# Kernel optimization log

Measured on AMD Instinct MI355X. Metric: run time of the kernel, lower is better.

The kernel has to match this reference:

```python
import jax, jax.numpy as jnp
import numpy as np

BLOCK_NUM = 64
B, M, K, N = 4, 4096, 4096, 4096  # batch, rows, in_features, out_features


def setup_inputs() -> dict:
    key = jax.random.key(0)
    k1, k2 = jax.random.split(key)
    x = jax.random.normal(k1, (B, M, K), dtype=jnp.float32)
    weight = jax.random.normal(k2, (K, N), dtype=jnp.float32) * 0.02
    return {"x": x, "weight": weight}


def reference(x, weight):
    # Block-local matmul: output block (i, j) = A_block(i, j) @ W_block(i, j).
    # No cross-block reduction: each (i, j) output block depends on exactly one
    # A block and one W block. Vectorized as a single einsum over all blocks.
    b, m, k = x.shape
    k2, n = weight.shape
    Bn = BLOCK_NUM
    r, c, o = m // Bn, k // Bn, n // Bn  # per-block rows / contract / cols
    A = x.reshape(b, Bn, r, Bn, c)        # [b, i, r, j, c]
    W = weight.reshape(Bn, c, Bn, o)      # [i, c, j, o] (rows split by i, cols by j)
    out = jnp.einsum('birjc,icjo->birjo', A, W)
    return out.reshape(b, m, n)
```

## Files before the change

### kernel.cpp

```cpp
#include <hip/hip_runtime.h>
#include <hip/hip_bf16.h>


typedef short bf16x8 __attribute__((ext_vector_type(8)));
typedef float f32x4 __attribute__((ext_vector_type(4)));

__device__ __forceinline__ unsigned short f2bf(float f) {
    union { float f; unsigned int u; } v; v.f = f;
    unsigned int u = v.u;
    u += 0x7fffu + ((u >> 16) & 1u);
    return (unsigned short)(u >> 16);
}

__global__ __launch_bounds__(256, 4) void block_matmul_kernel(
    const float* __restrict__ x, const float* __restrict__ w,
    float* __restrict__ out) {
    __shared__ char smem[32768];
    unsigned short* Ws = reinterpret_cast<unsigned short*>(smem + 16384);
    float*          Os = reinterpret_cast<float*>(smem);

    const int chunk = 8192 >> 3;
    int orig = blockIdx.x;
    int wg   = (orig & 7) * chunk + (orig >> 3);

    int b = wg >> 11;
    int i = (wg >> 5) & 63;
    int q = wg & 31;

    const float* Ab = x   + ((size_t)(b * 4096 + i * 64)) * 4096 + q * 128;
    const float* Wb = w   + ((size_t)(i * 64)) * 4096 + q * 128;
    float*       Ob = out + ((size_t)(b * 4096 + i * 64)) * 4096 + q * 128;

    const int t = threadIdx.x;

    float4 va[8];
    #pragma unroll
    for (int it = 0; it < 8; ++it) {
        int idx = it * 256 + t;
        int m   = idx >> 5;
        int k4  = (idx & 31) << 2;
        va[it] = *reinterpret_cast<const float4*>(Ab + (size_t)m * 4096 + k4);
    }
    const int n  = t & 127;
    const int c0 = (t >> 7) << 2;
    float wv[32];
    #pragma unroll
    for (int it = 0; it < 8; ++it) {
        int c = it * 8 + c0;
        #pragma unroll
        for (int r = 0; r < 4; ++r)
            wv[it * 4 + r] = Wb[(size_t)(c + r) * 4096 + n];
    }

    #pragma unroll
    for (int it = 0; it < 8; ++it) {
        int idx = it * 256 + t;
        int m   = idx >> 5;
        int k4  = (idx & 31) << 2;
        unsigned long long pk =
            (unsigned long long)f2bf(va[it].x)         |
            ((unsigned long long)f2bf(va[it].y) << 16) |
            ((unsigned long long)f2bf(va[it].z) << 32) |
            ((unsigned long long)f2bf(va[it].w) << 48);
        int addr = m * 256 + ((k4 * 2) ^ ((m & 7) << 4));
        *reinterpret_cast<unsigned long long*>(smem + addr) = pk;
    }
    #pragma unroll
    for (int it = 0; it < 8; ++it) {
        int c = it * 8 + c0;
        unsigned long long pk =
            (unsigned long long)f2bf(wv[it * 4 + 0])         |
            ((unsigned long long)f2bf(wv[it * 4 + 1]) << 16) |
            ((unsigned long long)f2bf(wv[it * 4 + 2]) << 32) |
            ((unsigned long long)f2bf(wv[it * 4 + 3]) << 48);
        int addr = n * 128 + ((c * 2) ^ ((n & 7) << 4));
        *reinterpret_cast<unsigned long long*>(
            reinterpret_cast<char*>(Ws) + addr) = pk;
    }

    __syncthreads();

    const int l  = t & 63;
    const int wvid = t >> 6;
    const int lr = l & 15;
    const int lk = l >> 4;

    f32x4 acc[8];
    #pragma unroll
    for (int z = 0; z < 8; ++z) acc[z] = (f32x4){0.f, 0.f, 0.f, 0.f};

    const int am = wvid * 16 + lr;
    #pragma unroll
    for (int jj = 0; jj < 2; ++jj) {
        #pragma unroll
        for (int kt = 0; kt < 2; ++kt) {
            int kbA = jj * 128 + kt * 64 + lk * 16;
            bf16x8 af = *reinterpret_cast<const bf16x8*>(
                smem + am * 256 + (kbA ^ ((am & 7) << 4)));
            int kbB = kt * 64 + lk * 16;
            #pragma unroll
            for (int nt = 0; nt < 4; ++nt) {
                int bn = jj * 64 + nt * 16 + lr;
                bf16x8 bfr = *reinterpret_cast<const bf16x8*>(
                    reinterpret_cast<const char*>(Ws) + bn * 128 +
                    (kbB ^ ((bn & 7) << 4)));
                acc[jj * 4 + nt] =
                    __builtin_amdgcn_mfma_f32_16x16x32_bf16(af, bfr,
                                                            acc[jj * 4 + nt],
                                                            0, 0, 0);
            }
        }
    }

    __syncthreads();

    #pragma unroll
    for (int fn = 0; fn < 8; ++fn) {
        #pragma unroll
        for (int r = 0; r < 4; ++r) {
            int row = wvid * 16 + lk * 4 + r;
            int col = fn * 16 + lr;
            Os[row * 128 + (col ^ ((row & 7) << 2))] = acc[fn][r];
        }
    }

    __syncthreads();

    #pragma unroll
    for (int it = 0; it < 8; ++it) {
        int idx = it * 256 + t;
        int row = idx >> 5;
        int c4  = (idx & 31) << 2;
        int col = c4 ^ ((row & 7) << 2);
        f32x4 v = *reinterpret_cast<const f32x4*>(Os + row * 128 + col);
        *reinterpret_cast<f32x4*>(Ob + (size_t)row * 4096 + c4) = v;
    }
}

extern "C" void kernel_launch(void* const* d_in, const int* in_sizes, int n_in,
                              void* d_out, int out_size, void* d_ws, size_t ws_size,
                              hipStream_t stream) {
    const float* x = (const float*)d_in[0];
    const float* w = (const float*)d_in[1];
    float* out = (float*)d_out;

    dim3 grid(8192);
    dim3 block(256);
    block_matmul_kernel<<<grid, block, 0, stream>>>(x, w, out);
}
```

Measured before the change: 123.5 us.

## Reuse W tile across batch, load A straight to registers, prefetch next batch

```diff
diff --git a/kernel.cpp b/kernel.cpp
--- a/kernel.cpp
+++ b/kernel.cpp
@@ -12,67 +12,63 @@
     return (unsigned short)(u >> 16);
 }
 
+__device__ __forceinline__ bf16x8 pack8(float4 a, float4 b) {
+    bf16x8 r;
+    r[0] = (short)f2bf(a.x); r[1] = (short)f2bf(a.y);
+    r[2] = (short)f2bf(a.z); r[3] = (short)f2bf(a.w);
+    r[4] = (short)f2bf(b.x); r[5] = (short)f2bf(b.y);
+    r[6] = (short)f2bf(b.z); r[7] = (short)f2bf(b.w);
+    return r;
+}
+
 __global__ __launch_bounds__(256, 4) void block_matmul_kernel(
     const float* __restrict__ x, const float* __restrict__ w,
     float* __restrict__ out) {
-    __shared__ char smem[32768];
-    unsigned short* Ws = reinterpret_cast<unsigned short*>(smem + 16384);
-    float*          Os = reinterpret_cast<float*>(smem);
+    __shared__ unsigned short Ws[128 * 64];
 
-    const int chunk = 8192 >> 3;
     int orig = blockIdx.x;
-    int wg   = (orig & 7) * chunk + (orig >> 3);
-
-    int b = wg >> 11;
-    int i = (wg >> 5) & 63;
+    int wg   = (orig & 7) * 256 + (orig >> 3);
+    int i = wg >> 5;
     int q = wg & 31;
 
-    const float* Ab = x   + ((size_t)(b * 4096 + i * 64)) * 4096 + q * 128;
-    const float* Wb = w   + ((size_t)(i * 64)) * 4096 + q * 128;
-    float*       Ob = out + ((size_t)(b * 4096 + i * 64)) * 4096 + q * 128;
+    const float* Wb = w + (size_t)(i * 64) * 4096 + q * 128;
+    const size_t tile_off = (size_t)(i * 64) * 4096 + q * 128;
 
-    const int t = threadIdx.x;
+    const int t  = threadIdx.x;
+    const int l  = t & 63;
+    const int wv = t >> 6;
+    const int lr = l & 15;
+    const int lk = l >> 4;
+    const int am = wv * 16 + lr;
 
-    float4 va[8];
-    #pragma unroll
-    for (int it = 0; it < 8; ++it) {
-        int idx = it * 256 + t;
-        int m   = idx >> 5;
-        int k4  = (idx & 31) << 2;
-        va[it] = *reinterpret_cast<const float4*>(Ab + (size_t)m * 4096 + k4);
-    }
     const int n  = t & 127;
     const int c0 = (t >> 7) << 2;
-    float wv[32];
+    float wbuf[32];
     #pragma unroll
     for (int it = 0; it < 8; ++it) {
         int c = it * 8 + c0;
         #pragma unroll
         for (int r = 0; r < 4; ++r)
-            wv[it * 4 + r] = Wb[(size_t)(c + r) * 4096 + n];
+            wbuf[it * 4 + r] = Wb[(size_t)(c + r) * 4096 + n];
+    }
+
+    const float* Arow = x + tile_off + (size_t)am * 4096 + lk * 8;
+    float4 abuf[8];
+    #pragma unroll
+    for (int f = 0; f < 4; ++f) {
+        int off = (f >> 1) * 64 + (f & 1) * 32;
+        abuf[f * 2 + 0] = *reinterpret_cast<const float4*>(Arow + off);
+        abuf[f * 2 + 1] = *reinterpret_cast<const float4*>(Arow + off + 4);
     }
 
     #pragma unroll
     for (int it = 0; it < 8; ++it) {
-        int idx = it * 256 + t;
-        int m   = idx >> 5;
-        int k4  = (idx & 31) << 2;
-        unsigned long long pk =
-            (unsigned long long)f2bf(va[it].x)         |
-            ((unsigned long long)f2bf(va[it].y) << 16) |
-            ((unsigned long long)f2bf(va[it].z) << 32) |
-            ((unsigned long long)f2bf(va[it].w) << 48);
-        int addr = m * 256 + ((k4 * 2) ^ ((m & 7) << 4));
-        *reinterpret_cast<unsigned long long*>(smem + addr) = pk;
-    }
-    #pragma unroll
-    for (int it = 0; it < 8; ++it) {
         int c = it * 8 + c0;
         unsigned long long pk =
-            (unsigned long long)f2bf(wv[it * 4 + 0])         |
-            ((unsigned long long)f2bf(wv[it * 4 + 1]) << 16) |
-            ((unsigned long long)f2bf(wv[it * 4 + 2]) << 32) |
-            ((unsigned long long)f2bf(wv[it * 4 + 3]) << 48);
+            (unsigned long long)f2bf(wbuf[it * 4 + 0])         |
+            ((unsigned long long)f2bf(wbuf[it * 4 + 1]) << 16) |
+            ((unsigned long long)f2bf(wbuf[it * 4 + 2]) << 32) |
+            ((unsigned long long)f2bf(wbuf[it * 4 + 3]) << 48);
         int addr = n * 128 + ((c * 2) ^ ((n & 7) << 4));
         *reinterpret_cast<unsigned long long*>(
             reinterpret_cast<char*>(Ws) + addr) = pk;
@@ -80,60 +76,54 @@
 
     __syncthreads();
 
-    const int l  = t & 63;
-    const int wvid = t >> 6;
-    const int lr = l & 15;
-    const int lk = l >> 4;
+    #pragma unroll
+    for (int b = 0; b < 4; ++b) {
+        bf16x8 af[4];
+        #pragma unroll
+        for (int f = 0; f < 4; ++f)
+            af[f] = pack8(abuf[f * 2], abuf[f * 2 + 1]);
 
-    f32x4 acc[8];
-    #pragma unroll
-    for (int z = 0; z < 8; ++z) acc[z] = (f32x4){0.f, 0.f, 0.f, 0.f};
-
-    const int am = wvid * 16 + lr;
-    #pragma unroll
-    for (int jj = 0; jj < 2; ++jj) {
-        #pragma unroll
-        for (int kt = 0; kt < 2; ++kt) {
-            int kbA = jj * 128 + kt * 64 + lk * 16;
-            bf16x8 af = *reinterpret_cast<const bf16x8*>(
-                smem + am * 256 + (kbA ^ ((am & 7) << 4)));
-            int kbB = kt * 64 + lk * 16;
+        if (b < 3) {
+            const float* An = Arow + (size_t)(b + 1) * 4096 * 4096;
             #pragma unroll
-            for (int nt = 0; nt < 4; ++nt) {
-                int bn = jj * 64 + nt * 16 + lr;
-                bf16x8 bfr = *reinterpret_cast<const bf16x8*>(
-                    reinterpret_cast<const char*>(Ws) + bn * 128 +
-                    (kbB ^ ((bn & 7) << 4)));
-                acc[jj * 4 + nt] =
-                    __builtin_amdgcn_mfma_f32_16x16x32_bf16(af, bfr,
-                                                            acc[jj * 4 + nt],
-                                                            0, 0, 0);
+            for (int f = 0; f < 4; ++f) {
+                int off = (f >> 1) * 64 + (f & 1) * 32;
+                abuf[f * 2 + 0] = *reinterpret_cast<const float4*>(An + off);
+                abuf[f * 2 + 1] = *reinterpret_cast<const float4*>(An + off + 4);
             }
         }
-    }
 
-    __syncthreads();
+        f32x4 acc[8];
+        #pragma unroll
+        for (int z = 0; z < 8; ++z) acc[z] = (f32x4){0.f, 0.f, 0.f, 0.f};
+        #pragma unroll
+        for (int jj = 0; jj < 2; ++jj) {
+            #pragma unroll
+            for (int kt = 0; kt < 2; ++kt) {
+                bf16x8 a = af[jj * 2 + kt];
+                int kbB = kt * 64 + lk * 16;
+                #pragma unroll
+                for (int nt = 0; nt < 4; ++nt) {
+                    int bn = jj * 64 + nt * 16 + lr;
+                    bf16x8 bfr = *reinterpret_cast<const bf16x8*>(
+                        reinterpret_cast<const char*>(Ws) + bn * 128 +
+                        (kbB ^ ((bn & 7) << 4)));
+                    acc[jj * 4 + nt] = __builtin_amdgcn_mfma_f32_16x16x32_bf16(
+                        a, bfr, acc[jj * 4 + nt], 0, 0, 0);
+                }
+            }
+        }
 
-    #pragma unroll
-    for (int fn = 0; fn < 8; ++fn) {
+        float* Ob = out + (size_t)b * 4096 * 4096 + tile_off;
         #pragma unroll
-        for (int r = 0; r < 4; ++r) {
-            int row = wvid * 16 + lk * 4 + r;
-            int col = fn * 16 + lr;
-            Os[row * 128 + (col ^ ((row & 7) << 2))] = acc[fn][r];
+        for (int fn = 0; fn < 8; ++fn) {
+            #pragma unroll
+            for (int r = 0; r < 4; ++r) {
+                int orow = wv * 16 + lk * 4 + r;
+                int ocol = fn * 16 + lr;
+                Ob[(size_t)orow * 4096 + ocol] = acc[fn][r];
+            }
         }
-    }
-
-    __syncthreads();
-
-    #pragma unroll
-    for (int it = 0; it < 8; ++it) {
-        int idx = it * 256 + t;
-        int row = idx >> 5;
-        int c4  = (idx & 31) << 2;
-        int col = c4 ^ ((row & 7) << 2);
-        f32x4 v = *reinterpret_cast<const f32x4*>(Os + row * 128 + col);
-        *reinterpret_cast<f32x4*>(Ob + (size_t)row * 4096 + c4) = v;
     }
 }
 
@@ -144,7 +134,7 @@
     const float* w = (const float*)d_in[1];
     float* out = (float*)d_out;
 
-    dim3 grid(8192);
+    dim3 grid(2048);
     dim3 block(256);
     block_matmul_kernel<<<grid, block, 0, stream>>>(x, w, out);
 }
```

Result: slower. 136.7 us (+10.8%).
